# Optimization experiments

Hardware: AMD Instinct MI355X
Metric: run time of the kernel (lower is better)

## Reference

```python
import jax, jax.numpy as jnp
import numpy as np

N_NODES = 100000
N_EDGES = 1600000
EPS = 1e-5
ALPHA = 0.01  # leaky relu slope


def gcn_conv(x, src, dst, W, b, n_nodes):
    """PyG GCNConv: h = W x, add self-loops, out = D^-1/2 (A+I) D^-1/2 h + b."""
    h = x @ W  # [N, d_out]
    # add self loops
    loop = jnp.arange(n_nodes, dtype=src.dtype)
    s = jnp.concatenate([src, loop])
    d = jnp.concatenate([dst, loop])
    # symmetric normalization: deg computed at destination over A + I
    deg = jax.ops.segment_sum(jnp.ones_like(d, dtype=h.dtype), d, num_segments=n_nodes)
    dinv = jnp.where(deg > 0, jax.lax.rsqrt(deg), 0.0)
    norm = dinv[s] * dinv[d]  # [E+N]
    msg = h[s] * norm[:, None]  # gather + scale (memory bound)
    out = jax.ops.segment_sum(msg, d, num_segments=n_nodes)
    return out + b


def batch_norm(x, gamma, beta):
    mu = jnp.mean(x, axis=0)
    var = jnp.var(x, axis=0)
    return (x - mu) * jax.lax.rsqrt(var + EPS) * gamma + beta


def setup_inputs() -> dict:
    key = jax.random.key(0)
    ks = jax.random.split(key, 6)
    emb = jax.random.normal(ks[0], (N_NODES, 64), dtype=jnp.float32)
    edge_index = jax.random.randint(ks[1], (2, N_EDGES), 0, N_NODES, dtype=jnp.int32)
    W1 = jax.random.normal(ks[2], (64, 128), dtype=jnp.float32) * 0.05
    W2 = jax.random.normal(ks[3], (128, 256), dtype=jnp.float32) * 0.05
    Wf = jax.random.normal(ks[4], (256, 256), dtype=jnp.float32) * 0.05
    return {
        "embeddings": emb, "edge_index": edge_index,
        "W1": W1, "b1": jnp.zeros((128,), jnp.float32),
        "g1": jnp.ones((128,), jnp.float32), "beta1": jnp.zeros((128,), jnp.float32),
        "W2": W2, "b2": jnp.zeros((256,), jnp.float32),
        "g2": jnp.ones((256,), jnp.float32), "beta2": jnp.zeros((256,), jnp.float32),
        "Wf": Wf, "bf": jnp.zeros((256,), jnp.float32),
    }


def reference(embeddings, edge_index, W1, b1, g1, beta1, W2, b2, g2, beta2, Wf, bf):
    src, dst = edge_index[0], edge_index[1]
    x = gcn_conv(embeddings, src, dst, W1, b1, N_NODES)
    x = batch_norm(x, g1, beta1)
    x = jnp.where(x >= 0, x, ALPHA * x)  # leaky relu; dropout = identity (eval)
    x = gcn_conv(x, src, dst, W2, b2, N_NODES)
    x = batch_norm(x, g2, beta2)
    x = jnp.where(x >= 0, x, ALPHA * x)
    return x @ Wf + bf
```

## Files before the change

kernel.cpp:

```cpp
#include <hip/hip_runtime.h>

#define NN 100000
#define NE 1600000
constexpr float EPS_BN = 1e-5f;
constexpr float ALPHA = 0.01f;
constexpr int NBLK = (NN + 255) / 256;
constexpr int GBN = 128;
constexpr int NBUCK = (NN + 127) / 128;
constexpr int GA = 128;
constexpr int EPB = NE / GA;

typedef __attribute__((ext_vector_type(8))) short short8;
typedef __attribute__((ext_vector_type(4))) float f32x4;

__device__ __forceinline__ float bfu2f(uint lo16) {
    union { uint i; float f; } v; v.i = lo16 << 16; return v.f;
}
__device__ __forceinline__ float bfhi2f(uint u) {
    union { uint i; float f; } v; v.i = u & 0xffff0000u; return v.f;
}
__device__ __forceinline__ ushort f2bf(float f) {
    union { float f; uint i; } v; v.f = f;
    return (ushort)((v.i + 0x7fffu + ((v.i >> 16) & 1u)) >> 16);
}

__global__ __launch_bounds__(256) void k_bhist(const int* __restrict__ dstv, int* __restrict__ bcnt) {
    __shared__ int hist[NBUCK];
    for (int i = threadIdx.x; i < NBUCK; i += 256) hist[i] = 0;
    __syncthreads();
    int base = blockIdx.x * EPB;
    for (int i = threadIdx.x; i < EPB; i += 256)
        atomicAdd(&hist[dstv[base + i] >> 7], 1);
    __syncthreads();
    for (int i = threadIdx.x; i < NBUCK; i += 256)
        bcnt[i * GA + blockIdx.x] = hist[i];
}

__global__ __launch_bounds__(1024) void k_bscan(const int* __restrict__ bcnt,
                                                int* __restrict__ gcur, int* __restrict__ bbase) {
    __shared__ int tot[1024];
    int b = threadIdx.x;
    int t = 0;
    if (b < NBUCK)
        for (int k = 0; k < GA; ++k) t += bcnt[b * GA + k];
    tot[b] = t;
    __syncthreads();
    for (int off = 1; off < 1024; off <<= 1) {
        int u = (b >= off) ? tot[b - off] : 0;
        __syncthreads();
        tot[b] += u;
        __syncthreads();
    }
    int ex = tot[b] - t;
    if (b < NBUCK) {
        bbase[b] = ex;
        int cur = ex;
        for (int k = 0; k < GA; ++k) { gcur[b * GA + k] = cur; cur += bcnt[b * GA + k]; }
    }
    if (b == 0) bbase[NBUCK] = NE;
}

__global__ __launch_bounds__(256) void k_bscatter(const int* __restrict__ srcv, const int* __restrict__ dstv,
                                                  const int* __restrict__ gcur, uint* __restrict__ bpair) {
    __shared__ int lcur[NBUCK];
    for (int i = threadIdx.x; i < NBUCK; i += 256) lcur[i] = gcur[i * GA + blockIdx.x];
    __syncthreads();
    int base = blockIdx.x * EPB;
    for (int i = threadIdx.x; i < EPB; i += 256) {
        int d = dstv[base + i], s = srcv[base + i];
        int slot = atomicAdd(&lcur[d >> 7], 1);
        bpair[slot] = ((uint)(d & 127) << 17) | (uint)s;
    }
}

__global__ __launch_bounds__(256) void k_bcsr(const uint* __restrict__ bpair, const int* __restrict__ bbase,
                                              int* __restrict__ col, int* __restrict__ cnt,
                                              int* __restrict__ indptr) {
    __shared__ int h[128];
    __shared__ int off[128];
    int b = blockIdx.x, t = threadIdx.x;
    int p0 = bbase[b], p1 = bbase[b + 1];
    if (t < 128) h[t] = 0;
    __syncthreads();
    for (int i = p0 + t; i < p1; i += 256)
        atomicAdd(&h[bpair[i] >> 17], 1);
    __syncthreads();
    if (t < 128) off[t] = h[t];
    __syncthreads();
    for (int o = 1; o < 128; o <<= 1) {
        int u = 0;
        if (t < 128 && t >= o) u = off[t - o];
        __syncthreads();
        if (t < 128) off[t] += u;
        __syncthreads();
    }
    if (t < 128) {
        int st = p0 + off[t] - h[t];
        int node = b * 128 + t;
        if (node < NN) { indptr[node] = st; cnt[node] = h[t]; }
        off[t] = st;
    }
    __syncthreads();
    for (int i = p0 + t; i < p1; i += 256) {
        uint u = bpair[i];
        int slot = atomicAdd(&off[u >> 17], 1);
        col[slot] = (int)(u & 0x1FFFFu);
    }
}

__global__ void k_dinv(const int* __restrict__ cnt, float* __restrict__ dinv) {
    int i = blockIdx.x * 256 + threadIdx.x;
    if (i < NN) dinv[i] = rsqrtf((float)(cnt[i] + 1));
}

__global__ void k_wtrans(const float* __restrict__ W, ushort* __restrict__ WT, int K, int M) {
    int i = blockIdx.x * 256 + threadIdx.x;
    if (i < K * M) {
        int m = i / K, k = i % K;
        WT[i] = f2bf(W[(size_t)k * M + m]);
    }
}

__global__ __launch_bounds__(256) void k_semb(const float* __restrict__ emb, const float* __restrict__ dinv,
                                              uint2* __restrict__ embs) {
    int i = blockIdx.x * 256 + threadIdx.x;
    if (i >= NN * 16) return;
    int row = i >> 4;
    float dn = dinv[row];
    float4 f = ((const float4*)emb)[i];
    uint2 o;
    o.x = (uint)f2bf(f.x * dn) | ((uint)f2bf(f.y * dn) << 16);
    o.y = (uint)f2bf(f.z * dn) | ((uint)f2bf(f.w * dn) << 16);
    embs[i] = o;
}

__global__ __launch_bounds__(256) void k_x2s(const ushort* __restrict__ H1, const float* __restrict__ sc,
                                             const float* __restrict__ sh, const float* __restrict__ dinv,
                                             ushort* __restrict__ x2s) {
    int i = blockIdx.x * 256 + threadIdx.x;
    if (i >= NN * 16) return;
    int row = i >> 4, f0 = (i & 15) * 8;
    float dn = dinv[row];
    uint4 u = ((const uint4*)H1)[i];
    uint uu[4] = {u.x, u.y, u.z, u.w};
    uint oo[4];
#pragma unroll
    for (int q = 0; q < 4; ++q) {
        int f = f0 + q * 2;
        float e0 = bfu2f(uu[q] & 0xffffu) * sc[f] + sh[f];
        float e1 = bfhi2f(uu[q]) * sc[f + 1] + sh[f + 1];
        e0 = ((e0 >= 0.f) ? e0 : ALPHA * e0) * dn;
        e1 = ((e1 >= 0.f) ? e1 : ALPHA * e1) * dn;
        oo[q] = (uint)f2bf(e0) | ((uint)f2bf(e1) << 16);
    }
    uint4 o; o.x = oo[0]; o.y = oo[1]; o.z = oo[2]; o.w = oo[3];
    ((uint4*)x2s)[i] = o;
}

template <int W>
__global__ __launch_bounds__(64) void k_agg(const ushort* __restrict__ X, const int* __restrict__ indptr,
                                            const int* __restrict__ cnt, const int* __restrict__ col,
                                            const float* __restrict__ dinv, ushort* __restrict__ out) {
    int n = blockIdx.x, t = threadIdx.x;
    __shared__ int sc[64];
    int start = indptr[n], c = cnt[n];
    if constexpr (W == 64) {
        float a0 = bfu2f(X[(size_t)n * 64 + t]);
        for (int base = 0; base < c; base += 64) {
            int m = min(64, c - base);
            if (t < m) sc[t] = col[start + base + t];
            __syncthreads();
#pragma unroll 4
            for (int j = 0; j < m; ++j)
                a0 += bfu2f(X[(size_t)sc[j] * 64 + t]);
            __syncthreads();
        }
        out[(size_t)n * 64 + t] = f2bf(a0 * dinv[n]);
    } else {
        const uint* Xu = (const uint*)X;
        uint u = Xu[(size_t)n * 64 + t];
        float a0 = bfu2f(u & 0xffffu), a1 = bfhi2f(u);
        for (int base = 0; base < c; base += 64) {
            int m = min(64, c - base);
            if (t < m) sc[t] = col[start + base + t];
            __syncthreads();
#pragma unroll 4
            for (int j = 0; j < m; ++j) {
                uint v = Xu[(size_t)sc[j] * 64 + t];
                a0 += bfu2f(v & 0xffffu); a1 += bfhi2f(v);
            }
            __syncthreads();
        }
        float dn = dinv[n];
        ((uint*)out)[(size_t)n * 64 + t] = (uint)f2bf(a0 * dn) | ((uint)f2bf(a1 * dn) << 16);
    }
}

template <int K, int NOUT, int AT, int OUT>
__global__ __launch_bounds__(256) void k_mgemm(
        const void* __restrict__ Ap, const ushort* __restrict__ BT, void* __restrict__ Cp,
        const float* __restrict__ scale, const float* __restrict__ shift,
        const float* __restrict__ bias) {
    constexpr int BM = 128, BN = 64, BK = 32, LDA = 40;
    __shared__ ushort As[BM * LDA];
    __shared__ ushort Bs[BN * LDA];
    __shared__ float s_sc[K];
    __shared__ float s_sh[K];

    int tid = threadIdx.x;
    int brow = blockIdx.x * BM, bcol = blockIdx.y * BN;
    if constexpr (AT == 1) {
        for (int i = tid; i < K; i += 256) { s_sc[i] = scale[i]; s_sh[i] = shift[i]; }
        __syncthreads();
    }

    int lane = tid & 63, wid = tid >> 6;
    int wr = wid >> 1, wc = wid & 1;
    int fr = lane & 15, fq = lane >> 4;
    int fk = fq * 8;

    f32x4 acc[4][2];
#pragma unroll
    for (int mi = 0; mi < 4; ++mi)
#pragma unroll
        for (int ni = 0; ni < 2; ++ni) acc[mi][ni] = (f32x4){0.f, 0.f, 0.f, 0.f};

    const int srow = tid >> 1, sk0 = (tid & 1) * 16;
    const int grow = brow + srow;
    const bool aok = grow < NN;
    const int sbc = tid >> 2, sbk = (tid & 3) * 8;

    for (int kk = 0; kk < K; kk += BK) {
        __align__(16) ushort tmp[16];
#pragma unroll
        for (int j = 0; j < 16; ++j) tmp[j] = 0;
        if (aok) {
            const ushort* ap = (const ushort*)Ap + (size_t)grow * K + kk + sk0;
            if constexpr (AT == 2) {
                *(uint4*)&tmp[0] = *(const uint4*)ap;
                *(uint4*)&tmp[8] = *(const uint4*)(ap + 8);
            } else {
                uint4 u0 = *(const uint4*)ap;
                uint4 u1 = *(const uint4*)(ap + 8);
                uint uu[8] = {u0.x, u0.y, u0.z, u0.w, u1.x, u1.y, u1.z, u1.w};
#pragma unroll
                for (int q = 0; q < 8; ++q) {
                    int kq = kk + sk0 + q * 2;
                    float e0 = bfu2f(uu[q] & 0xffffu) * s_sc[kq] + s_sh[kq];
                    float e1 = bfhi2f(uu[q]) * s_sc[kq + 1] + s_sh[kq + 1];
                    e0 = (e0 >= 0.f) ? e0 : ALPHA * e0;
                    e1 = (e1 >= 0.f) ? e1 : ALPHA * e1;
                    tmp[q * 2 + 0] = f2bf(e0);
                    tmp[q * 2 + 1] = f2bf(e1);
                }
            }
        }
        *(uint4*)&As[srow * LDA + sk0] = *(uint4*)&tmp[0];
        *(uint4*)&As[srow * LDA + sk0 + 8] = *(uint4*)&tmp[8];

        uint4 ub = *(const uint4*)(BT + (size_t)(bcol + sbc) * K + kk + sbk);
        *(uint4*)&Bs[sbc * LDA + sbk] = ub;

        __syncthreads();

        short8 af[4], bfv[2];
#pragma unroll
        for (int mi = 0; mi < 4; ++mi)
            af[mi] = *(const short8*)&As[(wr * 64 + mi * 16 + fr) * LDA + fk];
#pragma unroll
        for (int ni = 0; ni < 2; ++ni)
            bfv[ni] = *(const short8*)&Bs[(wc * 32 + ni * 16 + fr) * LDA + fk];
#pragma unroll
        for (int mi = 0; mi < 4; ++mi)
#pragma unroll
            for (int ni = 0; ni < 2; ++ni)
                acc[mi][ni] = __builtin_amdgcn_mfma_f32_16x16x32_bf16(af[mi], bfv[ni], acc[mi][ni], 0, 0, 0);

        __syncthreads();
    }

    float bv[2];
#pragma unroll
    for (int ni = 0; ni < 2; ++ni) bv[ni] = bias[bcol + wc * 32 + ni * 16 + fr];

    if constexpr (OUT == 1) {
        float* outf = (float*)Cp;
#pragma unroll
        for (int mi = 0; mi < 4; ++mi)
#pragma unroll
            for (int r = 0; r < 4; ++r) {
                int row = brow + wr * 64 + mi * 16 + fq * 4 + r;
                if (row < NN) {
#pragma unroll
                    for (int ni = 0; ni < 2; ++ni) {
                        int c = bcol + wc * 32 + ni * 16 + fr;
                        outf[(size_t)row * NOUT + c] = acc[mi][ni][r] + bv[ni];
                    }
                }
            }
    } else {
        ushort* outb = (ushort*)Cp;
#pragma unroll
        for (int mi = 0; mi < 4; ++mi)
#pragma unroll
            for (int r = 0; r < 4; ++r) {
                int row = brow + wr * 64 + mi * 16 + fq * 4 + r;
                if (row < NN) {
#pragma unroll
                    for (int ni = 0; ni < 2; ++ni) {
                        int c = bcol + wc * 32 + ni * 16 + fr;
                        outb[(size_t)row * NOUT + c] = f2bf(acc[mi][ni][r] + bv[ni]);
                    }
                }
            }
    }
}

template <int M>
__global__ __launch_bounds__(256) void k_bnpart(const ushort* __restrict__ X, float* __restrict__ partials) {
    constexpr int FG = M / 4, RP = 256 / FG;
    __shared__ float rs[RP * M];
    __shared__ float rq[RP * M];
    int fg = threadIdx.x % FG, r0 = threadIdx.x / FG;
    float s0 = 0, s1 = 0, s2 = 0, s3 = 0, q0 = 0, q1 = 0, q2 = 0, q3 = 0;
    for (int n = blockIdx.x * RP + r0; n < NN; n += GBN * RP) {
        uint2 u = ((const uint2*)X)[(size_t)n * FG + fg];
        float v0 = bfu2f(u.x & 0xffffu), v1 = bfhi2f(u.x);
        float v2 = bfu2f(u.y & 0xffffu), v3 = bfhi2f(u.y);
        s0 += v0; q0 += v0 * v0;
        s1 += v1; q1 += v1 * v1;
        s2 += v2; q2 += v2 * v2;
        s3 += v3; q3 += v3 * v3;
    }
    int f0 = fg * 4;
    rs[r0 * M + f0 + 0] = s0; rq[r0 * M + f0 + 0] = q0;
    rs[r0 * M + f0 + 1] = s1; rq[r0 * M + f0 + 1] = q1;
    rs[r0 * M + f0 + 2] = s2; rq[r0 * M + f0 + 2] = q2;
    rs[r0 * M + f0 + 3] = s3; rq[r0 * M + f0 + 3] = q3;
    __syncthreads();
    for (int h = RP / 2; h; h >>= 1) {
        if (r0 < h) {
#pragma unroll
            for (int j = 0; j < 4; ++j) {
                rs[r0 * M + f0 + j] += rs[(r0 + h) * M + f0 + j];
                rq[r0 * M + f0 + j] += rq[(r0 + h) * M + f0 + j];
            }
        }
        __syncthreads();
    }
    if (threadIdx.x < M) {
        partials[(size_t)blockIdx.x * 2 * M + threadIdx.x] = rs[threadIdx.x];
        partials[(size_t)blockIdx.x * 2 * M + M + threadIdx.x] = rq[threadIdx.x];
    }
}

template <int M>
__global__ void k_bnred(const float* __restrict__ partials, const float* __restrict__ g,
                        const float* __restrict__ be, float* __restrict__ scale,
                        float* __restrict__ shift) {
    int f = threadIdx.x;
    if (f < M) {
        float s = 0.f, q = 0.f;
        for (int b = 0; b < GBN; ++b) {
            s += partials[(size_t)b * 2 * M + f];
            q += partials[(size_t)b * 2 * M + M + f];
        }
        float mu = s * (1.f / NN);
        float var = q * (1.f / NN) - mu * mu;
        float r = rsqrtf(var + EPS_BN);
        float sc = g[f] * r;
        scale[f] = sc;
        shift[f] = be[f] - mu * sc;
    }
}

extern "C" void kernel_launch(void* const* d_in, const int* in_sizes, int n_in,
                              void* d_out, int out_size, void* d_ws, size_t ws_size,
                              hipStream_t stream) {
    const float* emb = (const float*)d_in[0];
    const int* eidx  = (const int*)d_in[1];
    const float* W1  = (const float*)d_in[2];
    const float* b1  = (const float*)d_in[3];
    const float* g1  = (const float*)d_in[4];
    const float* be1 = (const float*)d_in[5];
    const float* W2  = (const float*)d_in[6];
    const float* b2  = (const float*)d_in[7];
    const float* g2  = (const float*)d_in[8];
    const float* be2 = (const float*)d_in[9];
    const float* Wf  = (const float*)d_in[10];
    const float* bf  = (const float*)d_in[11];
    float* out = (float*)d_out;
    const int* srcv = eidx;
    const int* dstv = eidx + NE;

    char* w = (char*)d_ws;
    auto alloc = [&](size_t bytes) {
        char* p = w;
        w += (bytes + 255) / 256 * 256;
        return p;
    };
    int* cnt    = (int*)alloc((size_t)NN * 4);
    int* indptr = (int*)alloc((size_t)NN * 4);
    int* bcnt   = (int*)alloc((size_t)NBUCK * GA * 4);
    int* gcur   = (int*)alloc((size_t)NBUCK * GA * 4);
    int* bbase  = (int*)alloc((size_t)(NBUCK + 1) * 4);
    int* colb   = (int*)alloc((size_t)NE * 4);
    uint* bpair = (uint*)alloc((size_t)NE * 4);
    float* dinv = (float*)alloc((size_t)NN * 4);
    float* partials = (float*)alloc((size_t)GBN * 512 * 4);
    float* sc1 = (float*)alloc(128 * 4);
    float* sh1 = (float*)alloc(128 * 4);
    float* sc2 = (float*)alloc(256 * 4);
    float* sh2 = (float*)alloc(256 * 4);
    ushort* w1t = (ushort*)alloc((size_t)128 * 64 * 2);
    ushort* w2t = (ushort*)alloc((size_t)256 * 128 * 2);
    ushort* wft = (ushort*)alloc((size_t)256 * 256 * 2);
    ushort* slabA = (ushort*)alloc((size_t)NN * 128 * 2);
    ushort* slabB = (ushort*)alloc((size_t)NN * 128 * 2);
    ushort* H2 = (ushort*)alloc((size_t)NN * 256 * 2);

    ushort* embs = slabA;
    ushort* aggE = slabB;
    ushort* H1   = slabA;
    ushort* x2s  = slabB;
    ushort* agg2 = slabA;

    k_bhist<<<GA, 256, 0, stream>>>(dstv, bcnt);
    k_bscan<<<1, 1024, 0, stream>>>(bcnt, gcur, bbase);
    k_bscatter<<<GA, 256, 0, stream>>>(srcv, dstv, gcur, bpair);
    k_bcsr<<<NBUCK, 256, 0, stream>>>(bpair, bbase, colb, cnt, indptr);
    k_dinv<<<NBLK, 256, 0, stream>>>(cnt, dinv);

    k_wtrans<<<(64 * 128 + 255) / 256, 256, 0, stream>>>(W1, w1t, 64, 128);
    k_wtrans<<<(128 * 256 + 255) / 256, 256, 0, stream>>>(W2, w2t, 128, 256);
    k_wtrans<<<(256 * 256 + 255) / 256, 256, 0, stream>>>(Wf, wft, 256, 256);

    constexpr int GX = (NN + 127) / 128;

    k_semb<<<(NN * 16 + 255) / 256, 256, 0, stream>>>(emb, dinv, (uint2*)embs);
    k_agg<64><<<NN, 64, 0, stream>>>(embs, indptr, cnt, colb, dinv, aggE);
    k_mgemm<64, 128, 2, 2><<<dim3(GX, 2), 256, 0, stream>>>(aggE, w1t, H1, nullptr, nullptr, b1);
    k_bnpart<128><<<GBN, 256, 0, stream>>>(H1, partials);
    k_bnred<128><<<1, 256, 0, stream>>>(partials, g1, be1, sc1, sh1);

    k_x2s<<<(NN * 16 + 255) / 256, 256, 0, stream>>>(H1, sc1, sh1, dinv, x2s);
    k_agg<128><<<NN, 64, 0, stream>>>(x2s, indptr, cnt, colb, dinv, agg2);
    k_mgemm<128, 256, 2, 2><<<dim3(GX, 4), 256, 0, stream>>>(agg2, w2t, H2, nullptr, nullptr, b2);
    k_bnpart<256><<<GBN, 256, 0, stream>>>(H2, partials);
    k_bnred<256><<<1, 256, 0, stream>>>(partials, g2, be2, sc2, sh2);

    k_mgemm<256, 256, 1, 1><<<dim3(GX, 4), 256, 0, stream>>>(H2, wft, out, sc2, sh2, bf);
}
```

Measured before the change: 432.1 us.

## Compute full output width per GEMM block, fuse small kernels, widen BN loads

The bf16 MFMA GEMM now computes all output columns per 128-row block instead of splitting columns across grid.y. The A tile (and, in the final GEMM, the BN+leaky-relu transform) is no longer loaded and recomputed once per column tile. The dinv computation is folded into the CSR build kernel, and the three weight-transpose launches are merged into one. The bucket-count layout is transposed for coalesced writes, and the BN partial reduction reads 16-byte vectors. The trade-off is more accumulators per wave and a larger B tile in shared memory, which can lower occupancy.

```diff
diff --git a/kernel.cpp b/kernel.cpp
--- a/kernel.cpp
+++ b/kernel.cpp
@@ -4,7 +4,6 @@
 #define NE 1600000
 constexpr float EPS_BN = 1e-5f;
 constexpr float ALPHA = 0.01f;
-constexpr int NBLK = (NN + 255) / 256;
 constexpr int GBN = 128;
 constexpr int NBUCK = (NN + 127) / 128;
 constexpr int GA = 128;
@@ -33,7 +32,7 @@
         atomicAdd(&hist[dstv[base + i] >> 7], 1);
     __syncthreads();
     for (int i = threadIdx.x; i < NBUCK; i += 256)
-        bcnt[i * GA + blockIdx.x] = hist[i];
+        bcnt[blockIdx.x * NBUCK + i] = hist[i];
 }
 
 __global__ __launch_bounds__(1024) void k_bscan(const int* __restrict__ bcnt,
@@ -42,7 +41,7 @@
     int b = threadIdx.x;
     int t = 0;
     if (b < NBUCK)
-        for (int k = 0; k < GA; ++k) t += bcnt[b * GA + k];
+        for (int k = 0; k < GA; ++k) t += bcnt[k * NBUCK + b];
     tot[b] = t;
     __syncthreads();
     for (int off = 1; off < 1024; off <<= 1) {
@@ -55,7 +54,7 @@
     if (b < NBUCK) {
         bbase[b] = ex;
         int cur = ex;
-        for (int k = 0; k < GA; ++k) { gcur[b * GA + k] = cur; cur += bcnt[b * GA + k]; }
+        for (int k = 0; k < GA; ++k) { gcur[k * NBUCK + b] = cur; cur += bcnt[k * NBUCK + b]; }
     }
     if (b == 0) bbase[NBUCK] = NE;
 }
@@ -63,7 +62,7 @@
 __global__ __launch_bounds__(256) void k_bscatter(const int* __restrict__ srcv, const int* __restrict__ dstv,
                                                   const int* __restrict__ gcur, uint* __restrict__ bpair) {
     __shared__ int lcur[NBUCK];
-    for (int i = threadIdx.x; i < NBUCK; i += 256) lcur[i] = gcur[i * GA + blockIdx.x];
+    for (int i = threadIdx.x; i < NBUCK; i += 256) lcur[i] = gcur[blockIdx.x * NBUCK + i];
     __syncthreads();
     int base = blockIdx.x * EPB;
     for (int i = threadIdx.x; i < EPB; i += 256) {
@@ -75,7 +74,7 @@
 
 __global__ __launch_bounds__(256) void k_bcsr(const uint* __restrict__ bpair, const int* __restrict__ bbase,
                                               int* __restrict__ col, int* __restrict__ cnt,
-                                              int* __restrict__ indptr) {
+                                              int* __restrict__ indptr, float* __restrict__ dinv) {
     __shared__ int h[128];
     __shared__ int off[128];
     int b = blockIdx.x, t = threadIdx.x;
@@ -97,7 +96,11 @@
     if (t < 128) {
         int st = p0 + off[t] - h[t];
         int node = b * 128 + t;
-        if (node < NN) { indptr[node] = st; cnt[node] = h[t]; }
+        if (node < NN) {
+            indptr[node] = st;
+            cnt[node] = h[t];
+            dinv[node] = rsqrtf((float)(h[t] + 1));
+        }
         off[t] = st;
     }
     __syncthreads();
@@ -108,16 +111,21 @@
     }
 }
 
-__global__ void k_dinv(const int* __restrict__ cnt, float* __restrict__ dinv) {
+__global__ void k_wtrans_all(const float* __restrict__ W1, const float* __restrict__ W2,
+                             const float* __restrict__ Wf, ushort* __restrict__ w1t,
+                             ushort* __restrict__ w2t, ushort* __restrict__ wft) {
     int i = blockIdx.x * 256 + threadIdx.x;
-    if (i < NN) dinv[i] = rsqrtf((float)(cnt[i] + 1));
-}
-
-__global__ void k_wtrans(const float* __restrict__ W, ushort* __restrict__ WT, int K, int M) {
-    int i = blockIdx.x * 256 + threadIdx.x;
-    if (i < K * M) {
-        int m = i / K, k = i % K;
-        WT[i] = f2bf(W[(size_t)k * M + m]);
+    if (i < 8192) {
+        int m = i / 64, k = i % 64;
+        w1t[i] = f2bf(W1[(size_t)k * 128 + m]);
+    } else if (i < 8192 + 32768) {
+        int j = i - 8192;
+        int m = j / 128, k = j % 128;
+        w2t[j] = f2bf(W2[(size_t)k * 256 + m]);
+    } else if (i < 8192 + 32768 + 65536) {
+        int j = i - 8192 - 32768;
+        int m = j / 256, k = j % 256;
+        wft[j] = f2bf(Wf[(size_t)k * 256 + m]);
     }
 }
 
@@ -201,14 +209,16 @@
         const void* __restrict__ Ap, const ushort* __restrict__ BT, void* __restrict__ Cp,
         const float* __restrict__ scale, const float* __restrict__ shift,
         const float* __restrict__ bias) {
-    constexpr int BM = 128, BN = 64, BK = 32, LDA = 40;
+    constexpr int BM = 128, BK = 32, LDA = 40;
+    constexpr int WN = NOUT / 2;
+    constexpr int NF = WN / 16;
     __shared__ ushort As[BM * LDA];
-    __shared__ ushort Bs[BN * LDA];
+    __shared__ ushort Bs[NOUT * LDA];
     __shared__ float s_sc[K];
     __shared__ float s_sh[K];
 
     int tid = threadIdx.x;
-    int brow = blockIdx.x * BM, bcol = blockIdx.y * BN;
+    int brow = blockIdx.x * BM;
     if constexpr (AT == 1) {
         for (int i = tid; i < K; i += 256) { s_sc[i] = scale[i]; s_sh[i] = shift[i]; }
         __syncthreads();
@@ -219,16 +229,15 @@
     int fr = lane & 15, fq = lane >> 4;
     int fk = fq * 8;
 
-    f32x4 acc[4][2];
+    f32x4 acc[4][NF];
 #pragma unroll
     for (int mi = 0; mi < 4; ++mi)
 #pragma unroll
-        for (int ni = 0; ni < 2; ++ni) acc[mi][ni] = (f32x4){0.f, 0.f, 0.f, 0.f};
+        for (int ni = 0; ni < NF; ++ni) acc[mi][ni] = (f32x4){0.f, 0.f, 0.f, 0.f};
 
     const int srow = tid >> 1, sk0 = (tid & 1) * 16;
     const int grow = brow + srow;
     const bool aok = grow < NN;
-    const int sbc = tid >> 2, sbk = (tid & 3) * 8;
 
     for (int kk = 0; kk < K; kk += BK) {
         __align__(16) ushort tmp[16];
@@ -258,30 +267,34 @@
         *(uint4*)&As[srow * LDA + sk0] = *(uint4*)&tmp[0];
         *(uint4*)&As[srow * LDA + sk0 + 8] = *(uint4*)&tmp[8];
 
-        uint4 ub = *(const uint4*)(BT + (size_t)(bcol + sbc) * K + kk + sbk);
-        *(uint4*)&Bs[sbc * LDA + sbk] = ub;
-
-        __syncthreads();
-
-        short8 af[4], bfv[2];
+#pragma unroll
+        for (int it = 0; it < NOUT * BK / (256 * 8); ++it) {
+            int idx = tid + it * 256;
+            int bro = idx >> 2, bk = (idx & 3) * 8;
+            *(uint4*)&Bs[bro * LDA + bk] = *(const uint4*)(BT + (size_t)bro * K + kk + bk);
+        }
+
+        __syncthreads();
+
+        short8 af[4], bfv[NF];
 #pragma unroll
         for (int mi = 0; mi < 4; ++mi)
             af[mi] = *(const short8*)&As[(wr * 64 + mi * 16 + fr) * LDA + fk];
 #pragma unroll
-        for (int ni = 0; ni < 2; ++ni)
-            bfv[ni] = *(const short8*)&Bs[(wc * 32 + ni * 16 + fr) * LDA + fk];
+        for (int ni = 0; ni < NF; ++ni)
+            bfv[ni] = *(const short8*)&Bs[(wc * WN + ni * 16 + fr) * LDA + fk];
 #pragma unroll
         for (int mi = 0; mi < 4; ++mi)
 #pragma unroll
-            for (int ni = 0; ni < 2; ++ni)
+            for (int ni = 0; ni < NF; ++ni)
                 acc[mi][ni] = __builtin_amdgcn_mfma_f32_16x16x32_bf16(af[mi], bfv[ni], acc[mi][ni], 0, 0, 0);
 
         __syncthreads();
     }
 
-    float bv[2];
-#pragma unroll
-    for (int ni = 0; ni < 2; ++ni) bv[ni] = bias[bcol + wc * 32 + ni * 16 + fr];
+    float bv[NF];
+#pragma unroll
+    for (int ni = 0; ni < NF; ++ni) bv[ni] = bias[wc * WN + ni * 16 + fr];
 
     if constexpr (OUT == 1) {
         float* outf = (float*)Cp;
@@ -292,8 +305,8 @@
                 int row = brow + wr * 64 + mi * 16 + fq * 4 + r;
                 if (row < NN) {
 #pragma unroll
-                    for (int ni = 0; ni < 2; ++ni) {
-                        int c = bcol + wc * 32 + ni * 16 + fr;
+                    for (int ni = 0; ni < NF; ++ni) {
+                        int c = wc * WN + ni * 16 + fr;
                         outf[(size_t)row * NOUT + c] = acc[mi][ni][r] + bv[ni];
                     }
                 }
@@ -307,8 +320,8 @@
                 int row = brow + wr * 64 + mi * 16 + fq * 4 + r;
                 if (row < NN) {
 #pragma unroll
-                    for (int ni = 0; ni < 2; ++ni) {
-                        int c = bcol + wc * 32 + ni * 16 + fr;
+                    for (int ni = 0; ni < NF; ++ni) {
+                        int c = wc * WN + ni * 16 + fr;
                         outb[(size_t)row * NOUT + c] = f2bf(acc[mi][ni][r] + bv[ni]);
                     }
                 }
@@ -318,30 +331,32 @@
 
 template <int M>
 __global__ __launch_bounds__(256) void k_bnpart(const ushort* __restrict__ X, float* __restrict__ partials) {
-    constexpr int FG = M / 4, RP = 256 / FG;
+    constexpr int FG = M / 8, RP = 256 / FG;
     __shared__ float rs[RP * M];
     __shared__ float rq[RP * M];
     int fg = threadIdx.x % FG, r0 = threadIdx.x / FG;
-    float s0 = 0, s1 = 0, s2 = 0, s3 = 0, q0 = 0, q1 = 0, q2 = 0, q3 = 0;
+    float s[8] = {0, 0, 0, 0, 0, 0, 0, 0}, q[8] = {0, 0, 0, 0, 0, 0, 0, 0};
     for (int n = blockIdx.x * RP + r0; n < NN; n += GBN * RP) {
-        uint2 u = ((const uint2*)X)[(size_t)n * FG + fg];
-        float v0 = bfu2f(u.x & 0xffffu), v1 = bfhi2f(u.x);
-        float v2 = bfu2f(u.y & 0xffffu), v3 = bfhi2f(u.y);
-        s0 += v0; q0 += v0 * v0;
-        s1 += v1; q1 += v1 * v1;
-        s2 += v2; q2 += v2 * v2;
-        s3 += v3; q3 += v3 * v3;
-    }
-    int f0 = fg * 4;
-    rs[r0 * M + f0 + 0] = s0; rq[r0 * M + f0 + 0] = q0;
-    rs[r0 * M + f0 + 1] = s1; rq[r0 * M + f0 + 1] = q1;
-    rs[r0 * M + f0 + 2] = s2; rq[r0 * M + f0 + 2] = q2;
-    rs[r0 * M + f0 + 3] = s3; rq[r0 * M + f0 + 3] = q3;
+        uint4 u = ((const uint4*)X)[(size_t)n * FG + fg];
+        uint uu[4] = {u.x, u.y, u.z, u.w};
+#pragma unroll
+        for (int p = 0; p < 4; ++p) {
+            float v0 = bfu2f(uu[p] & 0xffffu), v1 = bfhi2f(uu[p]);
+            s[p * 2] += v0; q[p * 2] += v0 * v0;
+            s[p * 2 + 1] += v1; q[p * 2 + 1] += v1 * v1;
+        }
+    }
+    int f0 = fg * 8;
+#pragma unroll
+    for (int j = 0; j < 8; ++j) {
+        rs[r0 * M + f0 + j] = s[j];
+        rq[r0 * M + f0 + j] = q[j];
+    }
     __syncthreads();
     for (int h = RP / 2; h; h >>= 1) {
         if (r0 < h) {
 #pragma unroll
-            for (int j = 0; j < 4; ++j) {
+            for (int j = 0; j < 8; ++j) {
                 rs[r0 * M + f0 + j] += rs[(r0 + h) * M + f0 + j];
                 rq[r0 * M + f0 + j] += rq[(r0 + h) * M + f0 + j];
             }
@@ -428,26 +443,23 @@
     k_bhist<<<GA, 256, 0, stream>>>(dstv, bcnt);
     k_bscan<<<1, 1024, 0, stream>>>(bcnt, gcur, bbase);
     k_bscatter<<<GA, 256, 0, stream>>>(srcv, dstv, gcur, bpair);
-    k_bcsr<<<NBUCK, 256, 0, stream>>>(bpair, bbase, colb, cnt, indptr);
-    k_dinv<<<NBLK, 256, 0, stream>>>(cnt, dinv);
-
-    k_wtrans<<<(64 * 128 + 255) / 256, 256, 0, stream>>>(W1, w1t, 64, 128);
-    k_wtrans<<<(128 * 256 + 255) / 256, 256, 0, stream>>>(W2, w2t, 128, 256);
-    k_wtrans<<<(256 * 256 + 255) / 256, 256, 0, stream>>>(Wf, wft, 256, 256);
+    k_bcsr<<<NBUCK, 256, 0, stream>>>(bpair, bbase, colb, cnt, indptr, dinv);
+
+    k_wtrans_all<<<(8192 + 32768 + 65536 + 255) / 256, 256, 0, stream>>>(W1, W2, Wf, w1t, w2t, wft);
 
     constexpr int GX = (NN + 127) / 128;
 
     k_semb<<<(NN * 16 + 255) / 256, 256, 0, stream>>>(emb, dinv, (uint2*)embs);
     k_agg<64><<<NN, 64, 0, stream>>>(embs, indptr, cnt, colb, dinv, aggE);
-    k_mgemm<64, 128, 2, 2><<<dim3(GX, 2), 256, 0, stream>>>(aggE, w1t, H1, nullptr, nullptr, b1);
+    k_mgemm<64, 128, 2, 2><<<GX, 256, 0, stream>>>(aggE, w1t, H1, nullptr, nullptr, b1);
     k_bnpart<128><<<GBN, 256, 0, stream>>>(H1, partials);
     k_bnred<128><<<1, 256, 0, stream>>>(partials, g1, be1, sc1, sh1);
 
     k_x2s<<<(NN * 16 + 255) / 256, 256, 0, stream>>>(H1, sc1, sh1, dinv, x2s);
     k_agg<128><<<NN, 64, 0, stream>>>(x2s, indptr, cnt, colb, dinv, agg2);
-    k_mgemm<128, 256, 2, 2><<<dim3(GX, 4), 256, 0, stream>>>(agg2, w2t, H2, nullptr, nullptr, b2);
+    k_mgemm<128, 256, 2, 2><<<GX, 256, 0, stream>>>(agg2, w2t, H2, nullptr, nullptr, b2);
     k_bnpart<256><<<GBN, 256, 0, stream>>>(H2, partials);
     k_bnred<256><<<1, 256, 0, stream>>>(partials, g2, be2, sc2, sh2);
 
-    k_mgemm<256, 256, 1, 1><<<dim3(GX, 4), 256, 0, stream>>>(H2, wft, out, sc2, sh2, bf);
-}
+    k_mgemm<256, 256, 1, 1><<<GX, 256, 0, stream>>>(H2, wft, out, sc2, sh2, bf);
+}
```

New measurement: 382.2 us. -11.5%, faster.
